# Kernel tuning notes

Hardware: AMD Instinct MI355X
Metric: run time of the kernel (lower is better)

Reference implementation:

```python
import jax, jax.numpy as jnp
import numpy as np

B, L, D = 8, 8192, 256
H = 4 * D
EPS_LN = 1e-5
EPS_RELU = 1e-6
MIN_A, MAX_A, OFFSET = 0, 3, 3


def setup_inputs() -> dict:
    key = jax.random.key(0)
    ks = jax.random.split(key, 6)
    def n(k, shape, s=0.02):
        return jax.random.normal(k, shape, jnp.float32) * s
    return {
        "x": jax.random.normal(ks[0], (B, L, D), jnp.float32),
        "g1": jnp.ones((D,), jnp.float32), "b1": jnp.zeros((D,), jnp.float32),
        "g2": jnp.ones((D,), jnp.float32), "b2": jnp.zeros((D,), jnp.float32),
        "filt_w": n(ks[1], (L, D)),
        "w1": n(ks[2], (D, H)), "bb1": jnp.zeros((H,), jnp.float32),
        "w2": n(ks[3], (H, D)), "bb2": jnp.zeros((D,), jnp.float32),
    }


def layernorm(x, g, b):
    m = jnp.mean(x, -1, keepdims=True)
    v = jnp.var(x, -1, keepdims=True)
    return (x - m) * jax.lax.rsqrt(v + EPS_LN) * g + b


def maxpool_same(x, w):
    # stride-1 max pool over the last (frequency) axis, SAME padding
    if w == 1:
        return x
    return jax.lax.reduce_window(x, -jnp.inf, jax.lax.max,
                                 (1, 1, w), (1, 1, 1), "SAME")


def spsd1d(xt):
    """SPSD1D: FFT-based multi-scale (alpha) max-pooling spectral filter.
    xt: (B, D, L). Keeps rfft bins that are local maxima at every scale
    2**alpha for alpha in [MIN_A, MAX_A]; the lowest OFFSET bins pass through.
    Returns filtered signal (B, D, L) and argmax-alpha holder (B, D, F)."""
    X = jnp.fft.rfft(xt, axis=-1)              # (B, D, F), F = L//2 + 1
    mag = jnp.abs(X)
    pooled = jnp.stack([maxpool_same(mag, 2 ** a)
                        for a in range(MIN_A, MAX_A + 1)], 0)  # (A, B, D, F)
    max_holder = jnp.argmax(pooled, axis=0)
    env = jnp.max(pooled, axis=0)
    keep = (mag >= env) | (jnp.arange(mag.shape[-1]) < OFFSET)
    Xf = jnp.where(keep, X, 0.0)
    out = jnp.fft.irfft(Xf, n=xt.shape[-1], axis=-1)
    return out, max_holder


def _block_forward(x, g1, b1, g2, b2, filt_w, w1, bb1, w2, bb2):
    # EpsilonReLU(LayerNorm(x))
    h = jax.nn.relu(layernorm(x, g1, b1)) + EPS_RELU      # (B, L, D)
    # GlobalSPSDFilter: spsd over sequence axis, then elementwise weight
    f, _max_holder = spsd1d(jnp.swapaxes(h, 1, 2))        # (B, D, L)
    x0 = jnp.swapaxes(f, 1, 2) * filt_w                   # (B, L, D)
    # MLP(LayerNorm(x0)); dropouts are identity in eval mode
    m = layernorm(x0, g2, b2)
    m = jax.nn.gelu(m @ w1 + bb1, approximate=False)
    x0 = m @ w2 + bb2
    return x + x0


def reference(x, g1, b1, g2, b2, filt_w, w1, bb1, w2, bb2):
    return _block_forward(x, g1, b1, g2, b2, filt_w, w1, bb1, w2, bb2)
```

## Files before the change

### kernel.cpp

```cpp
#include <hip/hip_runtime.h>
#include <hip/hip_bf16.h>

#define BSZ  8
#define LSEQ 8192
#define DDIM 256
#define HDIM 1024
#define MFFT 4096

typedef __bf16 bf16;
typedef __bf16 bf16x8 __attribute__((ext_vector_type(8)));
typedef __bf16 bf16x4 __attribute__((ext_vector_type(4)));
typedef float  f32x4  __attribute__((ext_vector_type(4)));

__device__ __forceinline__ void wave_reduce2(float& a, float& b) {
    #pragma unroll
    for (int off = 1; off < 64; off <<= 1) {
        a += __shfl_xor(a, off);
        b += __shfl_xor(b, off);
    }
}

__device__ __forceinline__ void gl_lds16(const void* g, void* l) {
    __builtin_amdgcn_global_load_lds(
        (const __attribute__((address_space(1))) unsigned int*)(unsigned long long)g,
        (__attribute__((address_space(3))) unsigned int*)(unsigned int)(unsigned long long)l,
        16, 0, 0);
}

__global__ __launch_bounds__(256) void k0_prep(const float* __restrict__ w1,
                                               const float* __restrict__ w2,
                                               bf16* __restrict__ w1k,
                                               bf16* __restrict__ w2k,
                                               float2* __restrict__ tbl) {
    const int e = blockIdx.x * 256 + threadIdx.x;
    {
        const int c = e >> 14, r = e & 16383;
        const int ks = r >> 11, grp = (r >> 9) & 3, hh = (r >> 3) & 63, j = r & 7;
        w1k[e] = (bf16)w1[(ks * 32 + grp * 8 + j) * HDIM + c * 64 + hh];
    }
    {
        const int c = e >> 14, r = e & 16383;
        const int ks2 = r >> 13, grp = (r >> 11) & 3, d = (r >> 3) & 255, j = r & 7;
        w2k[e] = (bf16)w2[(c * 64 + ks2 * 32 + grp * 8 + j) * DDIM + d];
    }
    if (e <= 8184) {
        float ang;
        if (e < 3584) {
            const int f = e / 512 + 1, jj = e & 511;
            ang = -6.283185307179586f * (float)(f * jj) * (1.0f / 4096.0f);
        } else if (e < 4032) {
            const int t = e - 3584, f = t / 64 + 1, jj = t & 63;
            ang = -6.283185307179586f * (float)(f * jj) * (1.0f / 512.0f);
        } else if (e < 4088) {
            const int t = e - 4032, f = t / 8 + 1, jj = t & 7;
            ang = -6.283185307179586f * (float)(f * jj) * (1.0f / 64.0f);
        } else {
            const int k = e - 4088;
            ang = 3.14159265358979323846f * (float)k * (1.0f / 4096.0f);
        }
        tbl[e] = make_float2(cosf(ang), sinf(ang));
    }
}

__global__ __launch_bounds__(256) void k1_ln1_relu_T(const float* __restrict__ x,
                                                     const float* __restrict__ g1,
                                                     const float* __restrict__ b1,
                                                     float* __restrict__ ht) {
    __shared__ float tile[DDIM][33];
    const int tid  = threadIdx.x;
    const int wave = tid >> 6, lane = tid & 63;
    const int b  = blockIdx.x >> 8;
    const int l0 = (blockIdx.x & 255) << 5;
    const float4 g4 = *(const float4*)&g1[lane * 4];
    const float4 b4 = *(const float4*)&b1[lane * 4];
    for (int r8 = 0; r8 < 8; ++r8) {
        const int l = r8 * 4 + wave;
        const float4 v = *(const float4*)&x[(b * LSEQ + l0 + l) * DDIM + lane * 4];
        float s = v.x + v.y + v.z + v.w;
        float q = v.x * v.x + v.y * v.y + v.z * v.z + v.w * v.w;
        wave_reduce2(s, q);
        const float mean = s * (1.0f / 256.0f);
        const float var  = q * (1.0f / 256.0f) - mean * mean;
        const float rstd = rsqrtf(var + 1e-5f);
        const float vv[4] = {v.x, v.y, v.z, v.w};
        const float gg[4] = {g4.x, g4.y, g4.z, g4.w};
        const float bb[4] = {b4.x, b4.y, b4.z, b4.w};
        #pragma unroll
        for (int j = 0; j < 4; ++j) {
            float t = (vv[j] - mean) * rstd * gg[j] + bb[j];
            t = fmaxf(t, 0.0f) + 1e-6f;
            tile[lane * 4 + j][l] = t;
        }
    }
    __syncthreads();
    for (int i = tid; i < DDIM * 32; i += 256) {
        const int d = i >> 5, ll = i & 31;
        ht[(b * DDIM + d) * LSEQ + l0 + ll] = tile[d][ll];
    }
}

__device__ __forceinline__ int zs(int p) { return p ^ ((p >> 4) & 15); }
__device__ __forceinline__ float2 cmulf(float2 a, float2 b) {
    return make_float2(fmaf(a.x, b.x, -a.y * b.y), fmaf(a.x, b.y, a.y * b.x));
}
__device__ __forceinline__ float2 f2add(float2 a, float2 b) { return make_float2(a.x + b.x, a.y + b.y); }
__device__ __forceinline__ float2 f2sub(float2 a, float2 b) { return make_float2(a.x - b.x, a.y - b.y); }
#define CSQ2 0.70710678118654752440f

__device__ __forceinline__ void dft8(float2 a0, float2 a1, float2 a2, float2 a3,
                                     float2 a4, float2 a5, float2 a6, float2 a7,
                                     float2& y0, float2& y1, float2& y2, float2& y3,
                                     float2& y4, float2& y5, float2& y6, float2& y7) {
    const float2 s0 = f2add(a0, a4), s1 = f2add(a1, a5), s2 = f2add(a2, a6), s3 = f2add(a3, a7);
    const float2 d0 = f2sub(a0, a4), d1 = f2sub(a1, a5), d2 = f2sub(a2, a6), d3 = f2sub(a3, a7);
    const float2 d1t = make_float2(CSQ2 * (d1.x + d1.y), CSQ2 * (d1.y - d1.x));
    const float2 d2t = make_float2(d2.y, -d2.x);
    const float2 d3t = make_float2(CSQ2 * (d3.y - d3.x), -CSQ2 * (d3.x + d3.y));
    const float2 u0 = f2add(s0, s2), u1 = f2add(s1, s3);
    const float2 v0 = f2sub(s0, s2);
    const float2 sd = f2sub(s1, s3);
    const float2 v1 = make_float2(sd.y, -sd.x);
    const float2 e0 = f2add(d0, d2t), e1 = f2add(d1t, d3t);
    const float2 f0 = f2sub(d0, d2t);
    const float2 dd = f2sub(d1t, d3t);
    const float2 f1 = make_float2(dd.y, -dd.x);
    y0 = f2add(u0, u1); y4 = f2sub(u0, u1);
    y2 = f2add(v0, v1); y6 = f2sub(v0, v1);
    y1 = f2add(e0, e1); y5 = f2sub(e0, e1);
    y3 = f2add(f0, f1); y7 = f2sub(f0, f1);
}

template<int LQ, int TOFF>
__device__ __forceinline__ void stage8(float2* Z, const float2* __restrict__ tw, int tid) {
    const int q = 1 << LQ;
    const int j = tid & (q - 1);
    const int base = ((tid >> LQ) << (LQ + 3)) + j;
    const float2 a0 = Z[zs(base)],         a1 = Z[zs(base + q)];
    const float2 a2 = Z[zs(base + 2 * q)], a3 = Z[zs(base + 3 * q)];
    const float2 a4 = Z[zs(base + 4 * q)], a5 = Z[zs(base + 5 * q)];
    const float2 a6 = Z[zs(base + 6 * q)], a7 = Z[zs(base + 7 * q)];
    float2 y0, y1, y2, y3, y4, y5, y6, y7;
    dft8(a0, a1, a2, a3, a4, a5, a6, a7, y0, y1, y2, y3, y4, y5, y6, y7);
    y1 = cmulf(y1, tw[TOFF + j]);
    y2 = cmulf(y2, tw[TOFF + q + j]);
    y3 = cmulf(y3, tw[TOFF + 2 * q + j]);
    y4 = cmulf(y4, tw[TOFF + 3 * q + j]);
    y5 = cmulf(y5, tw[TOFF + 4 * q + j]);
    y6 = cmulf(y6, tw[TOFF + 5 * q + j]);
    y7 = cmulf(y7, tw[TOFF + 6 * q + j]);
    Z[zs(base)]         = y0;
    Z[zs(base + 4 * q)] = y1;
    Z[zs(base + 2 * q)] = y2;
    Z[zs(base + 6 * q)] = y3;
    Z[zs(base + q)]     = y4;
    Z[zs(base + 5 * q)] = y5;
    Z[zs(base + 3 * q)] = y6;
    Z[zs(base + 7 * q)] = y7;
    __syncthreads();
}

__device__ __forceinline__ void stage8_last(float2* Z, int tid) {
    const int base = tid << 3;
    const float2 a0 = Z[zs(base)],     a1 = Z[zs(base + 1)];
    const float2 a2 = Z[zs(base + 2)], a3 = Z[zs(base + 3)];
    const float2 a4 = Z[zs(base + 4)], a5 = Z[zs(base + 5)];
    const float2 a6 = Z[zs(base + 6)], a7 = Z[zs(base + 7)];
    __syncthreads();
    float2 y0, y1, y2, y3, y4, y5, y6, y7;
    dft8(a0, a1, a2, a3, a4, a5, a6, a7, y0, y1, y2, y3, y4, y5, y6, y7);
    const int r9 = (int)(__brev((unsigned)tid) >> 23);
    Z[zs(r9)]        = y0;
    Z[zs(512 + r9)]  = y1;
    Z[zs(1024 + r9)] = y2;
    Z[zs(1536 + r9)] = y3;
    Z[zs(2048 + r9)] = y4;
    Z[zs(2560 + r9)] = y5;
    Z[zs(3072 + r9)] = y6;
    Z[zs(3584 + r9)] = y7;
    __syncthreads();
}

__device__ __forceinline__ void fft4096(float2* Z, const float2* __restrict__ tw, int tid) {
    stage8<9, 0>(Z, tw, tid);
    stage8<6, 3584>(Z, tw, tid);
    stage8<3, 4032>(Z, tw, tid);
    stage8_last(Z, tid);
}

__global__ __launch_bounds__(512, 4) void k2_spsd(float* __restrict__ ht,
                                                  const float2* __restrict__ tw) {
    __shared__ float2 Z[MFFT];
    __shared__ float  mg[MFFT + 1];
    const int tid = threadIdx.x;
    float* row = ht + (size_t)blockIdx.x * LSEQ;
    const float2* U = tw + 4088;

    for (int m = tid; m < MFFT; m += 512)
        Z[zs(m)] = *(const float2*)&row[2 * m];
    __syncthreads();

    fft4096(Z, tw, tid);

    for (int k = tid; k <= MFFT; k += 512) {
        const int ka = k & (MFFT - 1);
        const int kb = (MFFT - k) & (MFFT - 1);
        const float2 A = Z[zs(ka)], Bc = Z[zs(kb)];
        const float zex = 0.5f * (A.x + Bc.x), zey = 0.5f * (A.y - Bc.y);
        const float zox = 0.5f * (A.y + Bc.y), zoy = -0.5f * (A.x - Bc.x);
        const float2 u = U[k];
        const float cs = u.x, sn = -u.y;
        const float xr = zex + zox * cs - zoy * sn;
        const float xi = zey + zox * sn + zoy * cs;
        mg[k] = sqrtf(xr * xr + xi * xi);
    }
    __syncthreads();

    for (int k = tid; k <= 2048; k += 512) {
        const int km = (MFFT - k) & (MFFT - 1);
        const float2 Pk = Z[zs(k)];
        const float2 Pm = Z[zs(km)];
        const float2 u = U[k];
        const float cs = u.x, sn = u.y;
        const float zex = 0.5f * (Pk.x + Pm.x), zey = 0.5f * (Pk.y - Pm.y);
        const float zox = 0.5f * (Pk.y + Pm.y), zoy = -0.5f * (Pk.x - Pm.x);
        float xkr = zex + zox * cs + zoy * sn;
        float xki = zey - zox * sn + zoy * cs;
        const float zex2 = 0.5f * (Pm.x + Pk.x), zey2 = 0.5f * (Pm.y - Pk.y);
        const float zox2 = 0.5f * (Pm.y + Pk.y), zoy2 = -0.5f * (Pm.x - Pk.x);
        float xmr = zex2 - zox2 * cs + zoy2 * sn;
        float xmi = zey2 - zox2 * sn - zoy2 * cs;
        const int jm = MFFT - k;
        bool keepk, keepm;
        {
            const int lo = (k - 3 < 0) ? 0 : k - 3;
            const int hi = (k + 4 > 4096) ? 4096 : k + 4;
            float mx = mg[k];
            for (int t2 = lo; t2 <= hi; ++t2) mx = fmaxf(mx, mg[t2]);
            keepk = (k < 3) || (mg[k] >= mx);
        }
        {
            const int hi = (jm + 4 > 4096) ? 4096 : jm + 4;
            float mx = mg[jm];
            for (int t2 = jm - 3; t2 <= hi; ++t2) mx = fmaxf(mx, mg[t2]);
            keepm = (mg[jm] >= mx);
        }
        if (!keepk) { xkr = 0.0f; xki = 0.0f; }
        if (!keepm) { xmr = 0.0f; xmi = 0.0f; }
        const float zpex = 0.5f * (xkr + xmr), zpey = 0.5f * (xki - xmi);
        const float dfx  = 0.5f * (xkr - xmr), dfy  = 0.5f * (xki + xmi);
        const float zpox = dfx * cs - dfy * sn, zpoy = dfx * sn + dfy * cs;
        const float2 zk = make_float2(zpex - zpoy, zpey + zpox);
        const float zex3 = 0.5f * (xmr + xkr), zey3 = 0.5f * (xmi - xki);
        const float df2x = 0.5f * (xmr - xkr), df2y = 0.5f * (xmi + xki);
        const float zo3x = -df2x * cs - df2y * sn, zo3y = df2x * sn - df2y * cs;
        const float2 zm = make_float2(zex3 - zo3y, zey3 + zo3x);
        Z[zs(k)] = make_float2(zk.x, -zk.y);
        if (k != 0 && k != 2048) Z[zs(MFFT - k)] = make_float2(zm.x, -zm.y);
    }
    __syncthreads();

    fft4096(Z, tw, tid);

    const float invM = 1.0f / (float)MFFT;
    for (int m = tid; m < MFFT; m += 512) {
        const float2 z = Z[zs(m)];
        *(float2*)&row[2 * m] = make_float2(z.x * invM, -z.y * invM);
    }
}

__global__ __launch_bounds__(256) void k3_filt_ln2(const float* __restrict__ ht,
                                                   const float* __restrict__ fw,
                                                   const float* __restrict__ g2,
                                                   const float* __restrict__ b2,
                                                   bf16* __restrict__ aln) {
    __shared__ float tile[DDIM][33];
    const int tid  = threadIdx.x;
    const int wave = tid >> 6, lane = tid & 63;
    const int b  = blockIdx.x >> 8;
    const int l0 = (blockIdx.x & 255) << 5;
    for (int i = tid; i < DDIM * 32; i += 256) {
        const int d = i >> 5, ll = i & 31;
        tile[d][ll] = ht[(b * DDIM + d) * LSEQ + l0 + ll];
    }
    __syncthreads();
    const float4 g4 = *(const float4*)&g2[lane * 4];
    const float4 bb4 = *(const float4*)&b2[lane * 4];
    for (int r8 = 0; r8 < 8; ++r8) {
        const int l = r8 * 4 + wave;
        const int gl = l0 + l;
        const float4 f4 = *(const float4*)&fw[gl * DDIM + lane * 4];
        float v[4];
        v[0] = tile[lane * 4 + 0][l] * f4.x;
        v[1] = tile[lane * 4 + 1][l] * f4.y;
        v[2] = tile[lane * 4 + 2][l] * f4.z;
        v[3] = tile[lane * 4 + 3][l] * f4.w;
        float s = v[0] + v[1] + v[2] + v[3];
        float q = v[0] * v[0] + v[1] * v[1] + v[2] * v[2] + v[3] * v[3];
        wave_reduce2(s, q);
        const float mean = s * (1.0f / 256.0f);
        const float var  = q * (1.0f / 256.0f) - mean * mean;
        const float rstd = rsqrtf(var + 1e-5f);
        const float gg[4] = {g4.x, g4.y, g4.z, g4.w};
        const float bb[4] = {bb4.x, bb4.y, bb4.z, bb4.w};
        bf16x4 o;
        #pragma unroll
        for (int j = 0; j < 4; ++j)
            o[j] = (bf16)((v[j] - mean) * rstd * gg[j] + bb[j]);
        *(bf16x4*)&aln[(b * LSEQ + gl) * DDIM + lane * 4] = o;
    }
}

#define LDS_W1 0
#define LDS_W2 32768
#define LDS_LM 65536
#define LDS_TOT 73728

__global__ __launch_bounds__(512, 4) void k4_mlp(const bf16* __restrict__ aln,
                                                 const bf16* __restrict__ w1k,
                                                 const bf16* __restrict__ w2k,
                                                 const float* __restrict__ bb1,
                                                 const float* __restrict__ bb2,
                                                 const float* __restrict__ x,
                                                 float* __restrict__ out) {
    extern __shared__ char sm[];
    const int tid = threadIdx.x;
    const int lane = tid & 63, w = tid >> 6;
    const int rowLane = lane & 15, grp = lane >> 4;
    const int wm = w >> 2, wn = w & 3;
    const int row0 = blockIdx.x << 6;

    bf16x8 aF[2][8];
    #pragma unroll
    for (int fm = 0; fm < 2; ++fm) {
        const size_t rb = (size_t)(row0 + wm * 32 + fm * 16 + rowLane) * DDIM;
        #pragma unroll
        for (int ks = 0; ks < 8; ++ks)
            aF[fm][ks] = *(const bf16x8*)(aln + rb + ks * 32 + grp * 8);
    }
    {
        const char* g1 = (const char*)w1k;
        #pragma unroll
        for (int r = 0; r < 4; ++r)
            gl_lds16(g1 + r * 8192 + tid * 16, sm + LDS_W1 + r * 8192 + tid * 16);
    }
    __syncthreads();

    f32x4 acc[2][4];
    #pragma unroll
    for (int i = 0; i < 2; ++i)
        #pragma unroll
        for (int j2 = 0; j2 < 4; ++j2) acc[i][j2] = (f32x4){0.f, 0.f, 0.f, 0.f};

    for (int c = 0; c < 16; ++c) {
        {
            const char* g2p = (const char*)w2k + (size_t)c * 32768;
            #pragma unroll
            for (int r = 0; r < 4; ++r)
                gl_lds16(g2p + r * 8192 + tid * 16, sm + LDS_W2 + r * 8192 + tid * 16);
        }
        const int hc = wn * 16 + rowLane;
        const float bias = bb1[c * 64 + hc];

        f32x4 p0 = {0.f, 0.f, 0.f, 0.f}, p1 = p0;
        #pragma unroll
        for (int ks = 0; ks < 8; ++ks) {
            const bf16x8 bF = *(const bf16x8*)(sm + LDS_W1 + ks * 4096 + grp * 1024 + hc * 16);
            p0 = __builtin_amdgcn_mfma_f32_16x16x32_bf16(aF[0][ks], bF, p0, 0, 0, 0);
            p1 = __builtin_amdgcn_mfma_f32_16x16x32_bf16(aF[1][ks], bF, p1, 0, 0, 0);
        }
        const int plane = ((hc >> 5) * 4 + ((hc >> 3) & 3)) * 1024 + (hc & 7) * 2;
        #pragma unroll
        for (int fm = 0; fm < 2; ++fm) {
            const f32x4 pv = fm ? p1 : p0;
            #pragma unroll
            for (int j = 0; j < 4; ++j) {
                const int prow = wm * 32 + fm * 16 + grp * 4 + j;
                const float v = pv[j] + bias;
                const float ge = 0.5f * v * (1.0f + erff(v * 0.70710678118654752f));
                *(bf16*)(sm + LDS_LM + plane + prow * 16) = (bf16)ge;
            }
        }
        __syncthreads();
        if (c < 15) {
            const char* g1 = (const char*)w1k + (size_t)(c + 1) * 32768;
            #pragma unroll
            for (int r = 0; r < 4; ++r)
                gl_lds16(g1 + r * 8192 + tid * 16, sm + LDS_W1 + r * 8192 + tid * 16);
        }
        #pragma unroll
        for (int ks2 = 0; ks2 < 2; ++ks2) {
            const bf16x8 a0 = *(const bf16x8*)(sm + LDS_LM + (ks2 * 4 + grp) * 1024 + (wm * 32 + rowLane) * 16);
            const bf16x8 a1 = *(const bf16x8*)(sm + LDS_LM + (ks2 * 4 + grp) * 1024 + (wm * 32 + 16 + rowLane) * 16);
            #pragma unroll
            for (int fn = 0; fn < 4; ++fn) {
                const int dcol = wn * 64 + fn * 16 + rowLane;
                const bf16x8 bw = *(const bf16x8*)(sm + LDS_W2 + (ks2 * 4 + grp) * 4096 + dcol * 16);
                acc[0][fn] = __builtin_amdgcn_mfma_f32_16x16x32_bf16(a0, bw, acc[0][fn], 0, 0, 0);
                acc[1][fn] = __builtin_amdgcn_mfma_f32_16x16x32_bf16(a1, bw, acc[1][fn], 0, 0, 0);
            }
        }
        __syncthreads();
    }
    #pragma unroll
    for (int fn = 0; fn < 4; ++fn) {
        const int dcol = wn * 64 + fn * 16 + rowLane;
        const float b2v = bb2[dcol];
        #pragma unroll
        for (int fm = 0; fm < 2; ++fm)
        #pragma unroll
        for (int j = 0; j < 4; ++j) {
            const int orow = row0 + wm * 32 + fm * 16 + grp * 4 + j;
            const int gi = orow * DDIM + dcol;
            out[gi] = acc[fm][fn][j] + b2v + x[gi];
        }
    }
}

extern "C" void kernel_launch(void* const* d_in, const int* in_sizes, int n_in,
                              void* d_out, int out_size, void* d_ws, size_t ws_size,
                              hipStream_t stream) {
    (void)in_sizes; (void)n_in; (void)out_size; (void)ws_size;
    const float* x   = (const float*)d_in[0];
    const float* g1  = (const float*)d_in[1];
    const float* b1  = (const float*)d_in[2];
    const float* g2  = (const float*)d_in[3];
    const float* b2  = (const float*)d_in[4];
    const float* fw  = (const float*)d_in[5];
    const float* w1  = (const float*)d_in[6];
    const float* bb1 = (const float*)d_in[7];
    const float* w2  = (const float*)d_in[8];
    const float* bb2 = (const float*)d_in[9];
    float* out = (float*)d_out;
    char*  ws  = (char*)d_ws;

    bf16*   aln = (bf16*)ws;
    bf16*   w1k = (bf16*)(ws + (size_t)33554432);
    bf16*   w2k = (bf16*)(ws + (size_t)34078720);
    float2* tbl = (float2*)(ws + (size_t)34603008);
    float* ht = out;

    k0_prep<<<dim3(1024), dim3(256), 0, stream>>>(w1, w2, w1k, w2k, tbl);
    k1_ln1_relu_T<<<dim3(2048), dim3(256), 0, stream>>>(x, g1, b1, ht);
    k2_spsd<<<dim3(2048), dim3(512), 0, stream>>>(ht, tbl);
    k3_filt_ln2<<<dim3(2048), dim3(256), 0, stream>>>(ht, fw, g2, b2, aln);
    k4_mlp<<<dim3(1024), dim3(512), LDS_TOT, stream>>>(aln, w1k, w2k, bb1, bb2, x, out);
}
```

Measured before the change: 280.0 us.

## Re-tile MLP kernel warps to 4x2 grid and pad GELU LDS staging buffer

```diff
diff --git a/kernel.cpp b/kernel.cpp
--- a/kernel.cpp
+++ b/kernel.cpp
@@ -313,7 +313,9 @@
 #define LDS_W1 0
 #define LDS_W2 32768
 #define LDS_LM 65536
-#define LDS_TOT 73728
+#define LDS_TOT 73984
+
+#define MFMA16 __builtin_amdgcn_mfma_f32_16x16x32_bf16
 
 __global__ __launch_bounds__(512, 4) void k4_mlp(const bf16* __restrict__ aln,
                                                  const bf16* __restrict__ w1k,
@@ -326,16 +328,15 @@
     const int tid = threadIdx.x;
     const int lane = tid & 63, w = tid >> 6;
     const int rowLane = lane & 15, grp = lane >> 4;
-    const int wm = w >> 2, wn = w & 3;
+    const int wm = w >> 1, wn = w & 1;
     const int row0 = blockIdx.x << 6;
 
-    bf16x8 aF[2][8];
-    #pragma unroll
-    for (int fm = 0; fm < 2; ++fm) {
-        const size_t rb = (size_t)(row0 + wm * 32 + fm * 16 + rowLane) * DDIM;
+    bf16x8 aF[8];
+    {
+        const size_t rb = (size_t)(row0 + wm * 16 + rowLane) * DDIM;
         #pragma unroll
         for (int ks = 0; ks < 8; ++ks)
-            aF[fm][ks] = *(const bf16x8*)(aln + rb + ks * 32 + grp * 8);
+            aF[ks] = *(const bf16x8*)(aln + rb + ks * 32 + grp * 8);
     }
     {
         const char* g1 = (const char*)w1k;
@@ -345,11 +346,9 @@
     }
     __syncthreads();
 
-    f32x4 acc[2][4];
+    f32x4 acc[8];
     #pragma unroll
-    for (int i = 0; i < 2; ++i)
-        #pragma unroll
-        for (int j2 = 0; j2 < 4; ++j2) acc[i][j2] = (f32x4){0.f, 0.f, 0.f, 0.f};
+    for (int i = 0; i < 8; ++i) acc[i] = (f32x4){0.f, 0.f, 0.f, 0.f};
 
     for (int c = 0; c < 16; ++c) {
         {
@@ -358,26 +357,31 @@
             for (int r = 0; r < 4; ++r)
                 gl_lds16(g2p + r * 8192 + tid * 16, sm + LDS_W2 + r * 8192 + tid * 16);
         }
-        const int hc = wn * 16 + rowLane;
-        const float bias = bb1[c * 64 + hc];
+        const int hc0 = wn * 32 + rowLane;
 
         f32x4 p0 = {0.f, 0.f, 0.f, 0.f}, p1 = p0;
         #pragma unroll
         for (int ks = 0; ks < 8; ++ks) {
-            const bf16x8 bF = *(const bf16x8*)(sm + LDS_W1 + ks * 4096 + grp * 1024 + hc * 16);
-            p0 = __builtin_amdgcn_mfma_f32_16x16x32_bf16(aF[0][ks], bF, p0, 0, 0, 0);
-            p1 = __builtin_amdgcn_mfma_f32_16x16x32_bf16(aF[1][ks], bF, p1, 0, 0, 0);
-        }
-        const int plane = ((hc >> 5) * 4 + ((hc >> 3) & 3)) * 1024 + (hc & 7) * 2;
-        #pragma unroll
-        for (int fm = 0; fm < 2; ++fm) {
-            const f32x4 pv = fm ? p1 : p0;
+            const bf16x8 b0 = *(const bf16x8*)(sm + LDS_W1 + ks * 4096 + grp * 1024 + hc0 * 16);
+            const bf16x8 b1 = *(const bf16x8*)(sm + LDS_W1 + ks * 4096 + grp * 1024 + (hc0 + 16) * 16);
+            p0 = MFMA16(aF[ks], b0, p0, 0, 0, 0);
+            p1 = MFMA16(aF[ks], b1, p1, 0, 0, 0);
+        }
+        {
+            const float bias0 = bb1[c * 64 + hc0];
+            const float bias1 = bb1[c * 64 + hc0 + 16];
+            const int base0 = (hc0 >> 3) * 1056 + (hc0 & 7) * 2;
+            const int hc1 = hc0 + 16;
+            const int base1 = (hc1 >> 3) * 1056 + (hc1 & 7) * 2;
             #pragma unroll
             for (int j = 0; j < 4; ++j) {
-                const int prow = wm * 32 + fm * 16 + grp * 4 + j;
-                const float v = pv[j] + bias;
-                const float ge = 0.5f * v * (1.0f + erff(v * 0.70710678118654752f));
-                *(bf16*)(sm + LDS_LM + plane + prow * 16) = (bf16)ge;
+                const int prow = wm * 16 + grp * 4 + j;
+                const float v0 = p0[j] + bias0;
+                const float g0 = 0.5f * v0 * (1.0f + erff(v0 * 0.70710678118654752f));
+                *(bf16*)(sm + LDS_LM + base0 + prow * 16) = (bf16)g0;
+                const float v1 = p1[j] + bias1;
+                const float g1v = 0.5f * v1 * (1.0f + erff(v1 * 0.70710678118654752f));
+                *(bf16*)(sm + LDS_LM + base1 + prow * 16) = (bf16)g1v;
             }
         }
         __syncthreads();
@@ -389,29 +393,25 @@
         }
         #pragma unroll
         for (int ks2 = 0; ks2 < 2; ++ks2) {
-            const bf16x8 a0 = *(const bf16x8*)(sm + LDS_LM + (ks2 * 4 + grp) * 1024 + (wm * 32 + rowLane) * 16);
-            const bf16x8 a1 = *(const bf16x8*)(sm + LDS_LM + (ks2 * 4 + grp) * 1024 + (wm * 32 + 16 + rowLane) * 16);
+            const bf16x8 aM = *(const bf16x8*)(sm + LDS_LM + (ks2 * 4 + grp) * 1056 + (wm * 16 + rowLane) * 16);
             #pragma unroll
-            for (int fn = 0; fn < 4; ++fn) {
-                const int dcol = wn * 64 + fn * 16 + rowLane;
-                const bf16x8 bw = *(const bf16x8*)(sm + LDS_W2 + (ks2 * 4 + grp) * 4096 + dcol * 16);
-                acc[0][fn] = __builtin_amdgcn_mfma_f32_16x16x32_bf16(a0, bw, acc[0][fn], 0, 0, 0);
-                acc[1][fn] = __builtin_amdgcn_mfma_f32_16x16x32_bf16(a1, bw, acc[1][fn], 0, 0, 0);
+            for (int fn = 0; fn < 8; ++fn) {
+                const int dcol = wn * 128 + fn * 16 + rowLane;
+                const bf16x8 bw = *(const bf16x8*)(sm + LDS_W2 + ks2 * 16384 + grp * 4096 + dcol * 16);
+                acc[fn] = MFMA16(aM, bw, acc[fn], 0, 0, 0);
             }
         }
         __syncthreads();
     }
     #pragma unroll
-    for (int fn = 0; fn < 4; ++fn) {
-        const int dcol = wn * 64 + fn * 16 + rowLane;
+    for (int fn = 0; fn < 8; ++fn) {
+        const int dcol = wn * 128 + fn * 16 + rowLane;
         const float b2v = bb2[dcol];
         #pragma unroll
-        for (int fm = 0; fm < 2; ++fm)
-        #pragma unroll
         for (int j = 0; j < 4; ++j) {
-            const int orow = row0 + wm * 32 + fm * 16 + grp * 4 + j;
+            const int orow = row0 + wm * 16 + grp * 4 + j;
             const int gi = orow * DDIM + dcol;
-            out[gi] = acc[fm][fn][j] + b2v + x[gi];
+            out[gi] = acc[fn][j] + b2v + x[gi];
         }
     }
 }
```

After: 244.6 us. 12.7% less time.
